# Optimization experiments

Measured on AMD Instinct MI355X. Metric: run time of the kernel, lower is better.

## Reference

```python
import jax, jax.numpy as jnp
import numpy as np

B, N, E, Q = 4, 10000, 160000, 256
D, M, U, H, P = 128, 64, 126, 128, 7  # node_dim, msg_sz, update_sz, mlp hidden, pose dim
MSG_STEPS = 3
NUM_COPIES = 1


def setup_inputs() -> dict:
    key = jax.random.key(0)
    ks = jax.random.split(key, 12)
    return {
        "nodes_states": jax.random.normal(ks[0], (B, N, D), jnp.float32),
        "query_poses": jax.random.normal(ks[1], (B, Q, P), jnp.float32),
        "attn": jax.random.uniform(ks[2], (B, Q, N), jnp.float32) / N,
        "edge_sources": jax.random.randint(ks[3], (E,), 0, N),
        "edge_sinks": jax.random.randint(ks[4], (E,), 0, N),
        "w1e": jax.random.normal(ks[5], (2 * D, H), jnp.float32) * 0.05,
        "b1e": jnp.zeros((H,), jnp.float32),
        "w2e": jax.random.normal(ks[6], (H, M), jnp.float32) * 0.05,
        "b2e": jnp.zeros((M,), jnp.float32),
        "w1n": jax.random.normal(ks[7], (D + M, H), jnp.float32) * 0.05,
        "b1n": jnp.zeros((H,), jnp.float32),
        "w2n": jax.random.normal(ks[8], (H, U), jnp.float32) * 0.05,
        "b2n": jnp.zeros((U,), jnp.float32),
    }


def reference(nodes_states, query_poses, attn, edge_sources, edge_sinks,
              w1e, b1e, w2e, b2e, w1n, b1n, w2n, b2n):
    def step(states, _):
        # gather endpoint states: [B, E, 2*D]
        einp = jnp.concatenate([states[:, edge_sources], states[:, edge_sinks]], axis=-1)
        # edge MLP -> per-edge messages [B, E, M]
        msg = jax.nn.relu(einp @ w1e + b1e) @ w2e + b2e
        # scatter-add messages to sink nodes [B, N, M]
        incoming = jnp.zeros((states.shape[0], N, M), states.dtype).at[:, edge_sinks].add(msg)
        # node MLP update [B, N, U]
        ninp = jnp.concatenate([incoming, states], axis=-1)
        upd = jax.nn.relu(ninp @ w1n + b1n) @ w2n + b2n
        # only the last U channels (state part, not positions) are updated
        states = states.at[:, :, -U:].add(upd)
        return states, None

    states, _ = jax.lax.scan(step, nodes_states, None, length=MSG_STEPS)
    extraction = jnp.einsum('bqn,bnd->bqd', attn, states)  # interpolation readout
    return jnp.concatenate([query_poses] * NUM_COPIES + [extraction], axis=-1)
```

## Files before the change

### kernel.cpp

```cpp
#include <hip/hip_runtime.h>

#define Bx 4
#define Nn 10000
#define Ee 160000
#define Qq 256
#define Dd 128
#define Mm 64
#define Uu 126
#define Hh 128
#define Pp 7

#define KG 1252

typedef unsigned short u16;
typedef __bf16 bf16x8 __attribute__((ext_vector_type(8)));
typedef float f32x4 __attribute__((ext_vector_type(4)));

__device__ __forceinline__ float b2f(u16 h){
  unsigned u = ((unsigned)h) << 16; float f; __builtin_memcpy(&f, &u, 4); return f;
}
__device__ __forceinline__ u16 f2b(float f){
  __bf16 h = (__bf16)f; u16 r; __builtin_memcpy(&r, &h, 2); return r;
}
__device__ __forceinline__ float ldin(const void* p, long i, int flag){
  return flag ? b2f(((const u16*)p)[i]) : ((const float*)p)[i];
}

__global__ void probe_kernel(const void* in0, int* flag){
  if (threadIdx.x == 0 && blockIdx.x == 0){
    const u16* p = (const u16*)in0;
    int cnt = 0;
    for (int i = 0; i < 256; i++){
      float a = fabsf(b2f(p[i]));
      if (a > 0.0009765625f && a < 32.0f) cnt++;
    }
    *flag = (cnt >= 240) ? 1 : 0;
  }
}

__global__ void prep_init_kernel(const void* w1e, const void* b1e, const void* w2e, const void* b2e,
                                 const void* w1n, const void* b1n, const void* w2n, const void* b2n,
                                 const void* in0, const int* __restrict__ snk,
                                 const int* __restrict__ flag,
                                 u16* w1e_s, u16* w2e_s, u16* w1n_s, u16* w2n_s,
                                 float* b1e_f, float* b2e_f, float* b1n_f, float* b2n_f,
                                 float* __restrict__ sf, u16* __restrict__ sbm,
                                 int* __restrict__ cnt)
{
  int f = *flag;
  long gsz = (long)gridDim.x * blockDim.x;
  long base = (long)blockIdx.x * blockDim.x + threadIdx.x;
  for (long idx = base; idx < 82368; idx += gsz){
    if (idx < 32768){
      int k = (int)idx >> 7, h = (int)idx & 127;
      w1e_s[(k >> 3) * 1024 + h * 8 + (k & 7)] = f2b(ldin(w1e, idx, f));
    } else if (idx < 40960){
      int i2 = (int)idx - 32768; int k = i2 >> 6, m2 = i2 & 63;
      w2e_s[(k >> 3) * 512 + m2 * 8 + (k & 7)] = f2b(ldin(w2e, i2, f));
    } else if (idx < 65536){
      int i2 = (int)idx - 40960; int k = i2 >> 7, h = i2 & 127;
      w1n_s[(k >> 3) * 1024 + h * 8 + (k & 7)] = f2b(ldin(w1n, i2, f));
    } else if (idx < 81920){
      int i2 = (int)idx - 65536; int k = i2 >> 7, u = i2 & 127;
      float v = (u < 126) ? ldin(w2n, (long)k * 126 + u, f) : 0.f;
      w2n_s[(k >> 3) * 1024 + u * 8 + (k & 7)] = f2b(v);
    } else if (idx < 82048){ b1e_f[idx - 81920] = ldin(b1e, idx - 81920, f); }
    else if (idx < 82112){ b2e_f[idx - 82048] = ldin(b2e, idx - 82048, f); }
    else if (idx < 82240){ b1n_f[idx - 82112] = ldin(b1n, idx - 82112, f); }
    else { int j = (int)idx - 82240; b2n_f[j] = (j < 126) ? ldin(b2n, j, f) : 0.f; }
  }
  const long total = (long)Bx * Nn * Dd;
  for (long i = base; i < total; i += gsz){
    float v = ldin(in0, i, f);
    sf[i] = v; sbm[i] = f2b(v);
  }
  for (long i = base; i < Ee; i += gsz)
    atomicAdd(&cnt[snk[(int)i]], 1);
}

__global__ void scan_kernel(const int* __restrict__ cnt, int* __restrict__ rowp){
  __shared__ int tot[1024];
  int t = threadIdx.x;
  int base = t * 10;
  int local[10]; int s = 0;
  #pragma unroll
  for (int i = 0; i < 10; i++){
    int v = (base + i < Nn) ? cnt[base + i] : 0;
    local[i] = s; s += v;
  }
  tot[t] = s;
  __syncthreads();
  for (int o = 1; o < 1024; o <<= 1){
    int v = (t >= o) ? tot[t - o] : 0;
    __syncthreads();
    tot[t] += v;
    __syncthreads();
  }
  int prefix = (t == 0) ? 0 : tot[t - 1];
  #pragma unroll
  for (int i = 0; i < 10; i++)
    if (base + i < Nn) rowp[base + i] = prefix + local[i];
  if (t == 1023) rowp[Nn] = tot[1023];
}
__global__ void fill_kernel(const int* __restrict__ src, const int* __restrict__ snk,
                            const int* __restrict__ rowp, int* __restrict__ cnt,
                            int* __restrict__ psrc){
  int i = blockIdx.x * blockDim.x + threadIdx.x;
  if (i < Ee){
    int s = snk[i];
    int p = rowp[s] + atomicAdd(&cnt[s], 1);
    psrc[p] = src[i];
  }
}

__global__ __launch_bounds__(256) void xform_kernel(
  const u16* __restrict__ sbm, const u16* __restrict__ w1s,
  const float* __restrict__ b1f, u16* __restrict__ xab)
{
  __shared__ __align__(16) u16 w1h[16384];
  __shared__ __align__(16) u16 Yt[64 * 136];
  int tid = threadIdx.x;
  int b = (blockIdx.x & 7) >> 1;
  int nt = ((blockIdx.x >> 3) << 1) + (blockIdx.x & 1);
  if (nt >= 157) return;
  int n0 = nt * 64;
  int w = tid >> 6, lane = tid & 63, m = lane & 15, quad = lane >> 4;
  int n = n0 + w * 16 + m;
  int nld = n < Nn ? n : Nn - 1;
  const u16* srow = sbm + (((size_t)b * Nn + nld) << 7);

  bf16x8 a[4];
  #pragma unroll
  for (int lk = 0; lk < 4; lk++) a[lk] = *(const bf16x8*)(srow + lk * 32 + quad * 8);

  const f32x4 z4 = {0.f, 0.f, 0.f, 0.f};
  int row_l = lane >> 2, seg = lane & 3;
  int nst = n0 + w * 16 + row_l;

  #pragma unroll
  for (int half = 0; half < 2; half++){
    __syncthreads();
    {
      const uint4* g = (const uint4*)(w1s + half * 16384);
      uint4* l = (uint4*)w1h;
      #pragma unroll
      for (int i = 0; i < 8; i++) l[tid + i * 256] = g[tid + i * 256];
    }
    __syncthreads();
    f32x4 acc[8];
    #pragma unroll
    for (int ct = 0; ct < 8; ct++) acc[ct] = z4;
    #pragma unroll
    for (int lk = 0; lk < 4; lk++){
      #pragma unroll
      for (int ct = 0; ct < 8; ct++){
        bf16x8 bv = *(const bf16x8*)(w1h + (((lk * 4 + quad) << 7) + ct * 16 + m) * 8);
        acc[ct] = __builtin_amdgcn_mfma_f32_16x16x32_bf16(a[lk], bv, acc[ct], 0, 0, 0);
      }
    }
    #pragma unroll
    for (int ct = 0; ct < 8; ct++){
      float bb = (half == 0) ? b1f[ct * 16 + m] : 0.f;
      #pragma unroll
      for (int i = 0; i < 4; i++)
        Yt[(w * 16 + quad * 4 + i) * 136 + ct * 16 + m] = f2b(acc[ct][i] + bb);
    }
    if (nst < Nn){
      const u16* tb = Yt + (w * 16 + row_l) * 136 + seg * 8;
      uint4 x0 = *(const uint4*)(tb);
      uint4 x1 = *(const uint4*)(tb + 32);
      uint4 x2 = *(const uint4*)(tb + 64);
      uint4 x3 = *(const uint4*)(tb + 96);
      u16* gb = xab + ((size_t)b * Nn + nst) * 256 + half * 128 + seg * 8;
      *(uint4*)(gb)      = x0;
      *(uint4*)(gb + 32) = x1;
      *(uint4*)(gb + 64) = x2;
      *(uint4*)(gb + 96) = x3;
    }
  }
}

__global__ __launch_bounds__(256) void node_kernel(
  float* __restrict__ sf, u16* __restrict__ sbm, const u16* __restrict__ xab,
  const int* __restrict__ rowp, const int* __restrict__ psrc,
  const u16* __restrict__ w2es, const float* __restrict__ b2ef,
  const u16* __restrict__ w1s, const u16* __restrict__ w2s,
  const float* __restrict__ b1f, const float* __restrict__ b2f2)
{
  __shared__ __align__(16) u16 ninp[64 * 200];
  __shared__ __align__(16) u16 hsYt[64 * 136];
  int b = (blockIdx.x & 7) >> 1;
  int nt = ((blockIdx.x >> 3) << 1) + (blockIdx.x & 1);
  if (nt >= 157) return;
  int n0 = nt * 64;
  int tid = threadIdx.x;

  {
    int nl = tid >> 2, part = tid & 3;
    int n = n0 + nl;
    float acc[32];
    #pragma unroll
    for (int i = 0; i < 32; i++) acc[i] = 0.f;
    if (n < Nn){
      float xbf[32];
      {
        const u16* xp = xab + ((size_t)b * Nn + n) * 256 + 128 + part * 8;
        union { uint4 v; u16 h[8]; } q0, q1, q2, q3;
        q0.v = *(const uint4*)(xp);
        q1.v = *(const uint4*)(xp + 32);
        q2.v = *(const uint4*)(xp + 64);
        q3.v = *(const uint4*)(xp + 96);
        #pragma unroll
        for (int j = 0; j < 8; j++){
          xbf[j] = b2f(q0.h[j]); xbf[8 + j] = b2f(q1.h[j]);
          xbf[16 + j] = b2f(q2.h[j]); xbf[24 + j] = b2f(q3.h[j]);
        }
      }
      int r0 = rowp[n], r1 = rowp[n + 1];
      const u16* xb0 = xab + (size_t)b * Nn * 256 + part * 8;
      for (int r = r0; r < r1; r++){
        int s = psrc[r];
        const u16* xs = xb0 + (size_t)s * 256;
        union { uint4 v; u16 h[8]; } q0, q1, q2, q3;
        q0.v = *(const uint4*)(xs);
        q1.v = *(const uint4*)(xs + 32);
        q2.v = *(const uint4*)(xs + 64);
        q3.v = *(const uint4*)(xs + 96);
        #pragma unroll
        for (int j = 0; j < 8; j++){
          float v0 = b2f(q0.h[j]) + xbf[j];
          acc[j] += v0 > 0.f ? v0 : 0.f;
          float v1 = b2f(q1.h[j]) + xbf[8 + j];
          acc[8 + j] += v1 > 0.f ? v1 : 0.f;
          float v2 = b2f(q2.h[j]) + xbf[16 + j];
          acc[16 + j] += v2 > 0.f ? v2 : 0.f;
          float v3 = b2f(q3.h[j]) + xbf[24 + j];
          acc[24 + j] += v3 > 0.f ? v3 : 0.f;
        }
      }
    }
    union { u16 h[32]; uint4 v[4]; } hb;
    #pragma unroll
    for (int i = 0; i < 32; i++) hb.h[i] = f2b(acc[i]);
    u16* hp = hsYt + nl * 136 + part * 8;
    *(uint4*)(hp)      = hb.v[0];
    *(uint4*)(hp + 32) = hb.v[1];
    *(uint4*)(hp + 64) = hb.v[2];
    *(uint4*)(hp + 96) = hb.v[3];
    u16* dp = ninp + nl * 200 + 64 + part * 8;
    if (n < Nn){
      const u16* sp = sbm + (((size_t)b * Nn + n) << 7) + part * 8;
      *(uint4*)(dp)      = *(const uint4*)(sp);
      *(uint4*)(dp + 32) = *(const uint4*)(sp + 32);
      *(uint4*)(dp + 64) = *(const uint4*)(sp + 64);
      *(uint4*)(dp + 96) = *(const uint4*)(sp + 96);
    } else {
      uint4 zz = {0, 0, 0, 0};
      *(uint4*)(dp)      = zz;
      *(uint4*)(dp + 32) = zz;
      *(uint4*)(dp + 64) = zz;
      *(uint4*)(dp + 96) = zz;
    }
  }

  int w = tid >> 6, lane = tid & 63, m = lane & 15, quad = lane >> 4;
  const f32x4 z4 = {0.f, 0.f, 0.f, 0.f};

  {
    f32x4 acc[4];
    #pragma unroll
    for (int ct = 0; ct < 4; ct++) acc[ct] = z4;
    #pragma unroll
    for (int ks = 0; ks < 4; ks++){
      bf16x8 a = *(const bf16x8*)(hsYt + (w * 16 + m) * 136 + ks * 32 + quad * 8);
      #pragma unroll
      for (int ct = 0; ct < 4; ct++){
        bf16x8 bv = *(const bf16x8*)(w2es + (((ks * 4 + quad) << 6) + ct * 16 + m) * 8);
        acc[ct] = __builtin_amdgcn_mfma_f32_16x16x32_bf16(a, bv, acc[ct], 0, 0, 0);
      }
    }
    #pragma unroll
    for (int i = 0; i < 4; i++){
      int n = n0 + w * 16 + quad * 4 + i;
      float deg = (n < Nn) ? (float)(rowp[n + 1] - rowp[n]) : 0.f;
      #pragma unroll
      for (int ct = 0; ct < 4; ct++)
        ninp[(w * 16 + quad * 4 + i) * 200 + ct * 16 + m] = f2b(acc[ct][i] + deg * b2ef[ct * 16 + m]);
    }
  }

  f32x4 acc1[8];
  #pragma unroll
  for (int ct = 0; ct < 8; ct++) acc1[ct] = z4;
  #pragma unroll 1
  for (int ks = 0; ks < 6; ks++){
    bf16x8 a = *(const bf16x8*)(ninp + (w * 16 + m) * 200 + ks * 32 + quad * 8);
    #pragma unroll
    for (int ct = 0; ct < 8; ct++){
      bf16x8 bv = *(const bf16x8*)(w1s + (((ks * 4 + quad) << 7) + ct * 16 + m) * 8);
      acc1[ct] = __builtin_amdgcn_mfma_f32_16x16x32_bf16(a, bv, acc1[ct], 0, 0, 0);
    }
  }
  #pragma unroll
  for (int ct = 0; ct < 8; ct++){
    float bb = b1f[ct * 16 + m];
    #pragma unroll
    for (int i = 0; i < 4; i++){
      float v = acc1[ct][i] + bb;
      v = v > 0.f ? v : 0.f;
      hsYt[(w * 16 + quad * 4 + i) * 136 + ct * 16 + m] = f2b(v);
    }
  }
  f32x4 acc2[8];
  #pragma unroll
  for (int ct = 0; ct < 8; ct++) acc2[ct] = z4;
  #pragma unroll 1
  for (int ko = 0; ko < 4; ko++){
    bf16x8 a2 = *(const bf16x8*)(hsYt + (w * 16 + m) * 136 + ko * 32 + quad * 8);
    #pragma unroll
    for (int ct = 0; ct < 8; ct++){
      bf16x8 bv = *(const bf16x8*)(w2s + (((ko * 4 + quad) << 7) + ct * 16 + m) * 8);
      acc2[ct] = __builtin_amdgcn_mfma_f32_16x16x32_bf16(a2, bv, acc2[ct], 0, 0, 0);
    }
  }
  #pragma unroll
  for (int ct = 0; ct < 8; ct++){
    int u = ct * 16 + m;
    if (u < 126){
      float bb = b2f2[u];
      #pragma unroll
      for (int i = 0; i < 4; i++){
        int n = n0 + w * 16 + quad * 4 + i;
        if (n < Nn){
          size_t idx = (((size_t)b * Nn + n) << 7) + 2 + u;
          float v = sf[idx] + acc2[ct][i] + bb;
          sf[idx] = v;
          sbm[idx] = f2b(v);
        }
      }
    }
  }
}

__global__ __launch_bounds__(256) void swz_s_kernel(const u16* __restrict__ sbm, u16* __restrict__ sswz)
{
  __shared__ __align__(16) u16 tile[64 * 128];
  int blk = blockIdx.x;
  int b = blk & 3, nt = blk >> 2;
  int n0 = nt * 64;
  int t = threadIdx.x;
  {
    int row = t >> 2, s4 = (t & 3) * 4;
    int n = n0 + row;
    const uint4 z = {0, 0, 0, 0};
    const u16* gp = sbm + (((size_t)b * Nn + (n < Nn ? n : 0)) << 7);
    #pragma unroll
    for (int s = 0; s < 4; s++){
      uint4 v = (n < Nn) ? *(const uint4*)(gp + (s4 + s) * 8) : z;
      *(uint4*)(tile + row * 128 + (s4 + s) * 8) = v;
    }
  }
  __syncthreads();
  int kgl = t >> 5;
  int kg = nt * 8 + kgl;
  if (kg < KG){
    #pragma unroll
    for (int o = 0; o < 4; o++){
      int d = (t & 31) + o * 32;
      union { u16 h[8]; uint4 v[2]; } r;
      #pragma unroll
      for (int j = 0; j < 8; j++) r.h[j] = tile[(kgl * 8 + j) * 128 + d];
      u16* op = sswz + (((size_t)b * KG + kg) * 128 + d) * 8;
      *(uint4*)(op)     = r.v[0];
      *(uint4*)(op + 8) = r.v[1];
    }
  }
}
__global__ __launch_bounds__(256) void extract2_kernel(
  const void* __restrict__ attn, const int* __restrict__ flag,
  const u16* __restrict__ sswz, float* __restrict__ part)
{
  int f = *flag;
  int blk = blockIdx.x;
  int kc = blk & 31, qt = (blk >> 5) & 3, b = blk >> 7;
  int tid = threadIdx.x, w = tid >> 6, lane = tid & 63, m = lane & 15, quad = lane >> 4;
  int qr = qt * 4 + w, q0 = qr * 16;
  int kg0 = kc * 40;
  int nsteps = (kc == 31) ? 3 : 10;
  long arow = ((long)(b * Qq + q0 + m)) * Nn;
  const u16* ab16 = (const u16*)attn + arow;
  const float* af32 = (const float*)attn + arow;
  const u16* sbase = sswz + ((size_t)b) * KG * 1024;
  f32x4 acc[8];
  const f32x4 z4 = {0.f, 0.f, 0.f, 0.f};
  #pragma unroll
  for (int ct = 0; ct < 8; ct++) acc[ct] = z4;
  #pragma unroll 1
  for (int t = 0; t < nsteps; t++){
    int kg = kg0 + t * 4 + quad;
    int kgc = kg < KG ? kg : 0;
    bf16x8 a;
    if (kg < 1250){
      if (f){
        a = *(const bf16x8*)(ab16 + kg * 8);
      } else {
        const float* ap = af32 + kg * 8;
        float4 p0 = *(const float4*)ap;
        float4 p1 = *(const float4*)(ap + 4);
        a[0] = (__bf16)p0.x; a[1] = (__bf16)p0.y; a[2] = (__bf16)p0.z; a[3] = (__bf16)p0.w;
        a[4] = (__bf16)p1.x; a[5] = (__bf16)p1.y; a[6] = (__bf16)p1.z; a[7] = (__bf16)p1.w;
      }
    } else {
      #pragma unroll
      for (int j = 0; j < 8; j++) a[j] = (__bf16)0.f;
    }
    #pragma unroll
    for (int ct = 0; ct < 8; ct++){
      bf16x8 bv = *(const bf16x8*)(sbase + ((size_t)kgc * 128 + ct * 16 + m) * 8);
      acc[ct] = __builtin_amdgcn_mfma_f32_16x16x32_bf16(a, bv, acc[ct], 0, 0, 0);
    }
  }
  #pragma unroll
  for (int ct = 0; ct < 8; ct++){
    #pragma unroll
    for (int i = 0; i < 4; i++)
      part[(((size_t)(kc * 4 + b)) * Qq + q0 + quad * 4 + i) * 128 + ct * 16 + m] = acc[ct][i];
  }
}

__global__ void final_kernel(const void* __restrict__ poses, const int* __restrict__ flag,
                             const float* __restrict__ part, void* __restrict__ out)
{
  int f = *flag;
  const long total = (long)Bx * Qq * (Pp + Dd);
  for (long idx = (long)blockIdx.x * blockDim.x + threadIdx.x; idx < total; idx += (long)gridDim.x * blockDim.x){
    int j = (int)(idx % (Pp + Dd));
    long bq = idx / (Pp + Dd);
    float v;
    if (j < Pp){
      v = ldin(poses, bq * Pp + j, f);
    } else {
      int dd = j - Pp;
      int b = (int)(bq >> 8), q = (int)(bq & 255);
      v = 0.f;
      #pragma unroll
      for (int kc = 0; kc < 32; kc++)
        v += part[(((size_t)(kc * 4 + b) * Qq + q) << 7) + dd];
    }
    if (f) ((u16*)out)[idx] = f2b(v);
    else ((float*)out)[idx] = v;
  }
}

extern "C" void kernel_launch(void* const* d_in, const int* in_sizes, int n_in,
                              void* d_out, int out_size, void* d_ws, size_t ws_size,
                              hipStream_t stream)
{
  const void* in_states = d_in[0];
  const void* in_poses  = d_in[1];
  const void* in_attn   = d_in[2];
  const int*  in_src    = (const int*)d_in[3];
  const int*  in_snk    = (const int*)d_in[4];
  const void* in_w1e = d_in[5];  const void* in_b1e = d_in[6];
  const void* in_w2e = d_in[7];  const void* in_b2e = d_in[8];
  const void* in_w1n = d_in[9];  const void* in_b1n = d_in[10];
  const void* in_w2n = d_in[11]; const void* in_b2n = d_in[12];

  char* ws = (char*)d_ws;
  size_t off = 0;
  auto alloc = [&](size_t bytes){ size_t o = off; off = (off + bytes + 255) & ~(size_t)255; return o; };
  size_t o_sf   = alloc((size_t)Bx * Nn * Dd * 4);
  size_t o_sb   = alloc((size_t)Bx * Nn * Dd * 2);
  size_t o_xab  = alloc((size_t)Bx * Nn * 256 * 2);
  size_t o_rowp = alloc((size_t)(Nn + 1) * 4);
  size_t o_rcnt = alloc((size_t)Nn * 2 * 4);
  size_t o_psrc = alloc((size_t)Ee * 4);
  size_t o_w1e  = alloc(32768 * 2);
  size_t o_w2e  = alloc(8192 * 2);
  size_t o_w1n  = alloc(24576 * 2);
  size_t o_w2n  = alloc(16384 * 2);
  size_t o_b1e  = alloc(128 * 4);
  size_t o_b2e  = alloc(64 * 4);
  size_t o_b1n  = alloc(128 * 4);
  size_t o_b2n  = alloc(128 * 4);
  size_t o_flag = alloc(4);

  size_t sswzB = (size_t)Bx * KG * 128 * 8 * 2;
  size_t partB = (size_t)32 * Bx * Qq * Dd * 4;
  size_t o_sswz = alloc(sswzB);
  size_t o_part = alloc(partB);

  float* sf    = (float*)(ws + o_sf);
  u16*   sbm   = (u16*)(ws + o_sb);
  u16*   xab   = (u16*)(ws + o_xab);
  int*   rowp  = (int*)(ws + o_rowp);
  int*   rcnt  = (int*)(ws + o_rcnt);
  int*   rcnt2 = rcnt + Nn;
  int*   psrc  = (int*)(ws + o_psrc);
  u16*   w1e_s = (u16*)(ws + o_w1e);
  u16*   w2e_s = (u16*)(ws + o_w2e);
  u16*   w1n_s = (u16*)(ws + o_w1n);
  u16*   w2n_s = (u16*)(ws + o_w2n);
  float* b1e_f = (float*)(ws + o_b1e);
  float* b2e_f = (float*)(ws + o_b2e);
  float* b1n_f = (float*)(ws + o_b1n);
  float* b2n_f = (float*)(ws + o_b2n);
  int*   flag  = (int*)(ws + o_flag);
  u16*   sswz  = (u16*)(ws + o_sswz);
  float* part  = (float*)(ws + o_part);

  hipMemsetAsync(rcnt, 0, (size_t)Nn * 2 * 4, stream);
  probe_kernel<<<1, 64, 0, stream>>>(in_states, flag);
  prep_init_kernel<<<1024, 256, 0, stream>>>(in_w1e, in_b1e, in_w2e, in_b2e,
                                             in_w1n, in_b1n, in_w2n, in_b2n,
                                             in_states, in_snk, flag,
                                             w1e_s, w2e_s, w1n_s, w2n_s,
                                             b1e_f, b2e_f, b1n_f, b2n_f,
                                             sf, sbm, rcnt);
  scan_kernel<<<1, 1024, 0, stream>>>(rcnt, rowp);
  fill_kernel<<<(Ee + 255) / 256, 256, 0, stream>>>(in_src, in_snk, rowp, rcnt2, psrc);

  for (int step = 0; step < 3; step++){
    xform_kernel<<<632, 256, 0, stream>>>(sbm, w1e_s, b1e_f, xab);
    node_kernel<<<632, 256, 0, stream>>>(sf, sbm, xab, rowp, psrc,
                                         w2e_s, b2e_f,
                                         w1n_s, w2n_s, b1n_f, b2n_f);
  }
  swz_s_kernel<<<628, 256, 0, stream>>>(sbm, sswz);
  extract2_kernel<<<512, 256, 0, stream>>>(in_attn, flag, sswz, part);
  final_kernel<<<540, 256, 0, stream>>>(in_poses, flag, part, d_out);
}
```

Measured before the change: 358.1 us.

## Fuse final-step state swizzle into node kernel and parallelize dtype probe

```diff
diff --git a/kernel.cpp b/kernel.cpp
--- a/kernel.cpp
+++ b/kernel.cpp
@@ -27,15 +27,13 @@
 }
 
 __global__ void probe_kernel(const void* in0, int* flag){
-  if (threadIdx.x == 0 && blockIdx.x == 0){
-    const u16* p = (const u16*)in0;
-    int cnt = 0;
-    for (int i = 0; i < 256; i++){
-      float a = fabsf(b2f(p[i]));
-      if (a > 0.0009765625f && a < 32.0f) cnt++;
-    }
-    *flag = (cnt >= 240) ? 1 : 0;
-  }
+  __shared__ int cnt;
+  if (threadIdx.x == 0) cnt = 0;
+  __syncthreads();
+  float a = fabsf(b2f(((const u16*)in0)[threadIdx.x]));
+  if (a > 0.0009765625f && a < 32.0f) atomicAdd(&cnt, 1);
+  __syncthreads();
+  if (threadIdx.x == 0) *flag = (cnt >= 240) ? 1 : 0;
 }
 
 __global__ void prep_init_kernel(const void* w1e, const void* b1e, const void* w2e, const void* b2e,
@@ -185,7 +183,8 @@
   const int* __restrict__ rowp, const int* __restrict__ psrc,
   const u16* __restrict__ w2es, const float* __restrict__ b2ef,
   const u16* __restrict__ w1s, const u16* __restrict__ w2s,
-  const float* __restrict__ b1f, const float* __restrict__ b2f2)
+  const float* __restrict__ b1f, const float* __restrict__ b2f2,
+  u16* __restrict__ sswz, int last)
 {
   __shared__ __align__(16) u16 ninp[64 * 200];
   __shared__ __align__(16) u16 hsYt[64 * 136];
@@ -323,6 +322,7 @@
       acc2[ct] = __builtin_amdgcn_mfma_f32_16x16x32_bf16(a2, bv, acc2[ct], 0, 0, 0);
     }
   }
+
   #pragma unroll
   for (int ct = 0; ct < 8; ct++){
     int u = ct * 16 + m;
@@ -330,52 +330,48 @@
       float bb = b2f2[u];
       #pragma unroll
       for (int i = 0; i < 4; i++){
-        int n = n0 + w * 16 + quad * 4 + i;
+        int nl = w * 16 + quad * 4 + i;
+        int n = n0 + nl;
         if (n < Nn){
           size_t idx = (((size_t)b * Nn + n) << 7) + 2 + u;
           float v = sf[idx] + acc2[ct][i] + bb;
-          sf[idx] = v;
-          sbm[idx] = f2b(v);
+          if (!last){
+            sf[idx] = v;
+            sbm[idx] = f2b(v);
+          } else {
+            hsYt[nl * 136 + 2 + u] = f2b(v);
+          }
+        } else if (last){
+          hsYt[nl * 136 + 2 + u] = 0;
         }
       }
     }
   }
-}
-
-__global__ __launch_bounds__(256) void swz_s_kernel(const u16* __restrict__ sbm, u16* __restrict__ sswz)
-{
-  __shared__ __align__(16) u16 tile[64 * 128];
-  int blk = blockIdx.x;
-  int b = blk & 3, nt = blk >> 2;
-  int n0 = nt * 64;
-  int t = threadIdx.x;
-  {
-    int row = t >> 2, s4 = (t & 3) * 4;
-    int n = n0 + row;
-    const uint4 z = {0, 0, 0, 0};
-    const u16* gp = sbm + (((size_t)b * Nn + (n < Nn ? n : 0)) << 7);
-    #pragma unroll
-    for (int s = 0; s < 4; s++){
-      uint4 v = (n < Nn) ? *(const uint4*)(gp + (s4 + s) * 8) : z;
-      *(uint4*)(tile + row * 128 + (s4 + s) * 8) = v;
-    }
-  }
-  __syncthreads();
-  int kgl = t >> 5;
-  int kg = nt * 8 + kgl;
-  if (kg < KG){
-    #pragma unroll
-    for (int o = 0; o < 4; o++){
-      int d = (t & 31) + o * 32;
-      union { u16 h[8]; uint4 v[2]; } r;
-      #pragma unroll
-      for (int j = 0; j < 8; j++) r.h[j] = tile[(kgl * 8 + j) * 128 + d];
-      u16* op = sswz + (((size_t)b * KG + kg) * 128 + d) * 8;
-      *(uint4*)(op)     = r.v[0];
-      *(uint4*)(op + 8) = r.v[1];
-    }
-  }
-}
+  if (last){
+    if (m < 2){
+      #pragma unroll
+      for (int i = 0; i < 4; i++){
+        int nl = w * 16 + quad * 4 + i;
+        hsYt[nl * 136 + m] = ninp[nl * 200 + 64 + m];
+      }
+    }
+    #pragma unroll
+    for (int r = 0; r < 2; r++){
+      int kg = nt * 8 + w * 2 + r;
+      if (kg < KG){
+        #pragma unroll
+        for (int dd = 0; dd < 2; dd++){
+          int d = dd * 64 + lane;
+          union { u16 h[8]; uint4 v; } t;
+          #pragma unroll
+          for (int j = 0; j < 8; j++) t.h[j] = hsYt[(w * 16 + r * 8 + j) * 136 + d];
+          *(uint4*)(sswz + (((size_t)b * KG + kg) * 128 + d) * 8) = t.v;
+        }
+      }
+    }
+  }
+}
+
 __global__ __launch_bounds__(256) void extract2_kernel(
   const void* __restrict__ attn, const int* __restrict__ flag,
   const u16* __restrict__ sswz, float* __restrict__ part)
@@ -395,7 +391,7 @@
   const f32x4 z4 = {0.f, 0.f, 0.f, 0.f};
   #pragma unroll
   for (int ct = 0; ct < 8; ct++) acc[ct] = z4;
-  #pragma unroll 1
+  #pragma unroll 2
   for (int t = 0; t < nsteps; t++){
     int kg = kg0 + t * 4 + quad;
     int kgc = kg < KG ? kg : 0;
@@ -510,7 +506,7 @@
   float* part  = (float*)(ws + o_part);
 
   hipMemsetAsync(rcnt, 0, (size_t)Nn * 2 * 4, stream);
-  probe_kernel<<<1, 64, 0, stream>>>(in_states, flag);
+  probe_kernel<<<1, 256, 0, stream>>>(in_states, flag);
   prep_init_kernel<<<1024, 256, 0, stream>>>(in_w1e, in_b1e, in_w2e, in_b2e,
                                              in_w1n, in_b1n, in_w2n, in_b2n,
                                              in_states, in_snk, flag,
@@ -524,9 +520,9 @@
     xform_kernel<<<632, 256, 0, stream>>>(sbm, w1e_s, b1e_f, xab);
     node_kernel<<<632, 256, 0, stream>>>(sf, sbm, xab, rowp, psrc,
                                          w2e_s, b2e_f,
-                                         w1n_s, w2n_s, b1n_f, b2n_f);
-  }
-  swz_s_kernel<<<628, 256, 0, stream>>>(sbm, sswz);
+                                         w1n_s, w2n_s, b1n_f, b2n_f,
+                                         sswz, step == 2 ? 1 : 0);
+  }
   extract2_kernel<<<512, 256, 0, stream>>>(in_attn, flag, sswz, part);
   final_kernel<<<540, 256, 0, stream>>>(in_poses, flag, part, d_out);
 }
```

Result: faster. 347.5 us (-2.9%).
